# Optimization experiments

Measured on AMD Instinct MI355X. Metric: run time of the kernel, lower is better.

Reference implementation:

```python
import jax, jax.numpy as jnp
import numpy as np

B, T, D, H = 1024, 256, 8, 128


def setup_inputs() -> dict:
    key = jax.random.key(0)
    ks = jax.random.split(key, 8)
    def lin(k, fan_in, fan_out):
        # torch nn.Linear default init: U(-1/sqrt(fan_in), 1/sqrt(fan_in))
        bound = 1.0 / np.sqrt(fan_in)
        return jax.random.uniform(k, (fan_in, fan_out), jnp.float32, -bound, bound)
    return {
        "x": jax.random.normal(ks[0], (B, T, D), jnp.float32),
        "W_in": lin(ks[1], D, H), "b_in": jnp.zeros((H,), jnp.float32),
        "W0": lin(ks[2], H + 1, H), "b0": jnp.zeros((H,), jnp.float32),
        "W1": lin(ks[3], H, H), "b1": jnp.zeros((H,), jnp.float32),
        "W2": lin(ks[4], H, H * D), "b2": jnp.zeros((H * D,), jnp.float32),
    }


def _vector_field(t, z, W0, b0, W1, b1, W2, b2, hidden, inp):
    # inhomogeneous: append scalar time channel -> [B, H+1]
    h = jnp.concatenate([z, jnp.full((z.shape[0], 1), t, z.dtype)], axis=-1)
    h = jax.nn.relu(h @ W0 + b0)
    h = jax.nn.relu(h @ W1 + b1)          # num_layer = 1 extra hidden layer
    return jnp.tanh(h @ W2 + b2).reshape(-1, hidden, inp)  # [B, H, D]


def reference(x, W_in, b_in, W0, b0, W1, b1, W2, b2):
    b, t_len, d = x.shape
    hidden = W_in.shape[1]
    z0 = x[:, 0, :] @ W_in + b_in                     # init_states = input_layer(x[:,0])
    t_grid = jnp.linspace(0.0, 1.0, t_len)
    # linear interpolation of x on t_grid => dX/dt * dt over interval k is x[k+1]-x[k]
    dX = jnp.swapaxes(x[:, 1:, :] - x[:, :-1, :], 0, 1)  # [T-1, B, D]

    def step(z, inp):
        t_k, dx = inp
        F = _vector_field(t_k, z, W0, b0, W1, b1, W2, b2, hidden, d)
        z_next = z + jnp.einsum('bhd,bd->bh', F, dx)  # Euler step
        return z_next, z_next

    _, zs = jax.lax.scan(step, z0, (t_grid[:-1], dX))  # zs: [T-1, B, H]
    return jnp.concatenate([z0[:, None, :], jnp.swapaxes(zs, 0, 1)], axis=1)  # [B, T, H]
```

## Files before the change

### kernel.cpp

```cpp
#include <hip/hip_runtime.h>

#define TLEN 256
#define DD 8
#define HH 128
#define BR 16
#define NTHREADS 512

typedef __attribute__((ext_vector_type(8))) _Float16 half8;
typedef __attribute__((ext_vector_type(4))) float f32x4;

#define LOSCALE 65536.0f
#define LOINV   (1.0f/65536.0f)

static __device__ __forceinline__ float tanh_fast(float x){
  float cx = fminf(fmaxf(x, -9.01f), 9.01f);
  float e = __builtin_amdgcn_exp2f(cx * 2.885390081777927f);
  return 1.0f - 2.0f * __builtin_amdgcn_rcpf(e + 1.0f);
}

static __device__ __forceinline__ void split_store(float v, unsigned short* hiA, unsigned short* loA, unsigned byte){
  _Float16 h = (_Float16)v;
  _Float16 l = (_Float16)(v - (float)h);
  *(_Float16*)((char*)hiA + byte) = h;
  *(_Float16*)((char*)loA + byte) = l;
}

__global__ void pack_w2_kernel(const float* __restrict__ W2, half8* __restrict__ ws){
  int gid = blockIdx.x * 256 + threadIdx.x;
  int l = gid & 63;
  int f = gid >> 6;
  int kt = f & 3, ct = (f >> 2) & 7, w = f >> 5;
  int col = w*128 + ct*16 + (l & 15);
  int kb  = kt*32 + (l >> 4)*8;
  half8 vh, vl;
  #pragma unroll
  for (int j = 0; j < 8; j++){
    float v = W2[(kb + j)*1024 + col];
    _Float16 h = (_Float16)v;
    vh[j] = h;
    vl[j] = (_Float16)((v - (float)h) * LOSCALE);
  }
  ws[f*64 + l] = vh;
  ws[(256 + f)*64 + l] = vl;
}

__global__ __launch_bounds__(NTHREADS, 2) void ncde_kernel(
    const float* __restrict__ x, const float* __restrict__ Win, const float* __restrict__ bin,
    const float* __restrict__ W0, const float* __restrict__ b0v, const float* __restrict__ W1,
    const float* __restrict__ b1v, const float* __restrict__ W2, const float* __restrict__ b2v,
    const half8* __restrict__ wsw2, float* __restrict__ out)
{
  __shared__ half8 w0fh[2048], w0fl[2048];
  __shared__ half8 w1fh[2048], w1fl[2048];
  __shared__ unsigned short zhh[2048], zhl[2048];
  __shared__ unsigned short h1h[2048], h1l[2048];
  __shared__ unsigned short h2h[2048], h2l[2048];
  __shared__ f32x4 b2lds4[256];

  const int t    = threadIdx.x;
  const int lane = t & 63;
  const int w    = t >> 6;
  const int lg   = lane >> 4;
  const int ln   = lane & 15;
  const int b0blk = blockIdx.x * BR;
  const int dbase = (lg & 1) * 4;

  for (int s = t; s < 4096; s += NTHREADS){
    int which = s >> 11;
    int s2 = s & 2047;
    int la = s2 & 63;
    int nt = (s2 >> 6) & 7;
    int kt = s2 >> 9;
    const float* Wsrc = which ? W1 : W0;
    int kb  = kt*32 + (la >> 4)*8;
    int col = nt*16 + (la & 15);
    half8 vh, vl;
    #pragma unroll
    for (int j = 0; j < 8; j++){
      float v = Wsrc[(kb + j)*HH + col];
      _Float16 h = (_Float16)v;
      vh[j] = h;
      vl[j] = (_Float16)((v - (float)h) * LOSCALE);
    }
    if (which){ w1fh[s2] = vh; w1fl[s2] = vl; } else { w0fh[s2] = vh; w0fl[s2] = vl; }
  }
  for (int s = t; s < 1024; s += NTHREADS) ((float*)b2lds4)[s] = b2v[s];

  half8 w2f[8][4];
  #pragma unroll
  for (int ct = 0; ct < 8; ct++)
    #pragma unroll
    for (int kt = 0; kt < 4; kt++)
      w2f[ct][kt] = wsw2[((w*8 + ct)*4 + kt)*64 + lane];
  const half8* wsL = wsw2 + 256*64;

  const float b0r = b0v[w*16 + ln];
  const float w0L = W0[128*HH + w*16 + ln];
  const float b1r = b1v[w*16 + ln];

  f32x4 xprev = *(const f32x4*)(x + (size_t)(b0blk + ln)*(TLEN*DD) + dbase);

  for (int o = t; o < BR*HH; o += NTHREADS){
    int br = o >> 7, h = o & 127;
    float acc = bin[h];
    const float* xb = x + (size_t)(b0blk + br)*(TLEN*DD);
    #pragma unroll
    for (int d = 0; d < DD; d++) acc += xb[d] * Win[d*HH + h];
    unsigned byte = (unsigned)br*256u + (((unsigned)h*2u) ^ (((unsigned)(br & 7)) << 4));
    split_store(acc, zhh, zhl, byte);
  }
  __syncthreads();

  float zreg[8];
  #pragma unroll
  for (int ct = 0; ct < 8; ct++){
    int h = w*16 + ct*2 + (lg >> 1);
    unsigned byte = (unsigned)ln*256u + (((unsigned)h*2u) ^ (((unsigned)(ln & 7)) << 4));
    zreg[ct] = (float)*(_Float16*)((char*)zhh + byte) + (float)*(_Float16*)((char*)zhl + byte);
  }

  float* outp[4];
  #pragma unroll
  for (int i = 0; i < 4; i++){
    int o = t + i*NTHREADS;
    int br = o >> 7, h = o & 127;
    outp[i] = out + (size_t)(b0blk + br)*(TLEN*HH) + h;
    unsigned byte = (unsigned)br*256u + (((unsigned)h*2u) ^ (((unsigned)(br & 7)) << 4));
    *outp[i] = (float)*(_Float16*)((char*)zhh + byte) + (float)*(_Float16*)((char*)zhl + byte);
    outp[i] += HH;
  }

  const float inv = 1.0f / 255.0f;

  for (int k = 0; k < TLEN - 1; k++){
    float tk = (float)k * inv;

    f32x4 xn = *(const f32x4*)(x + (size_t)(b0blk + ln)*(TLEN*DD) + (size_t)(k + 1)*DD + dbase);

    f32x4 acch = {0.f,0.f,0.f,0.f}, accl = {0.f,0.f,0.f,0.f}, acc2 = {0.f,0.f,0.f,0.f};
    #pragma unroll
    for (int kt = 0; kt < 4; kt++){
      unsigned byte = (unsigned)ln*256u + ((((unsigned)(kt*4 + lg))*16u) ^ (((unsigned)(ln & 7)) << 4));
      half8 ahi = *(const half8*)((const char*)zhh + byte);
      half8 alo = *(const half8*)((const char*)zhl + byte);
      half8 bh = w0fh[(kt*8 + w)*64 + lane];
      half8 bl = w0fl[(kt*8 + w)*64 + lane];
      acch = __builtin_amdgcn_mfma_f32_16x16x32_f16(ahi, bh, acch, 0, 0, 0);
      accl = __builtin_amdgcn_mfma_f32_16x16x32_f16(alo, bh, accl, 0, 0, 0);
      acc2 = __builtin_amdgcn_mfma_f32_16x16x32_f16(ahi, bl, acc2, 0, 0, 0);
    }
    {
      float c0 = b0r + tk * w0L;
      #pragma unroll
      for (int r = 0; r < 4; r++){
        float v = fmaxf(acch[r] + accl[r] + acc2[r]*LOINV + c0, 0.0f);
        int row = lg*4 + r;
        unsigned byte = (unsigned)row*256u + ((((unsigned)(w*16 + ln))*2u) ^ (((unsigned)(row & 7)) << 4));
        split_store(v, h1h, h1l, byte);
      }
    }
    __syncthreads();

    acch = (f32x4){0.f,0.f,0.f,0.f}; accl = (f32x4){0.f,0.f,0.f,0.f}; acc2 = (f32x4){0.f,0.f,0.f,0.f};
    #pragma unroll
    for (int kt = 0; kt < 4; kt++){
      unsigned byte = (unsigned)ln*256u + ((((unsigned)(kt*4 + lg))*16u) ^ (((unsigned)(ln & 7)) << 4));
      half8 ahi = *(const half8*)((const char*)h1h + byte);
      half8 alo = *(const half8*)((const char*)h1l + byte);
      half8 bh = w1fh[(kt*8 + w)*64 + lane];
      half8 bl = w1fl[(kt*8 + w)*64 + lane];
      acch = __builtin_amdgcn_mfma_f32_16x16x32_f16(ahi, bh, acch, 0, 0, 0);
      accl = __builtin_amdgcn_mfma_f32_16x16x32_f16(alo, bh, accl, 0, 0, 0);
      acc2 = __builtin_amdgcn_mfma_f32_16x16x32_f16(ahi, bl, acc2, 0, 0, 0);
    }
    #pragma unroll
    for (int r = 0; r < 4; r++){
      float v = fmaxf(acch[r] + accl[r] + acc2[r]*LOINV + b1r, 0.0f);
      int row = lg*4 + r;
      unsigned byte = (unsigned)row*256u + ((((unsigned)(w*16 + ln))*2u) ^ (((unsigned)(row & 7)) << 4));
      split_store(v, h2h, h2l, byte);
    }
    half8 wl[4];
    #pragma unroll
    for (int kt = 0; kt < 4; kt++) wl[kt] = wsL[((w*8 + 0)*4 + kt)*64 + lane];
    __syncthreads();

    half8 ahh[4], ahl[4];
    #pragma unroll
    for (int kt = 0; kt < 4; kt++){
      unsigned byte = (unsigned)ln*256u + ((((unsigned)(kt*4 + lg))*16u) ^ (((unsigned)(ln & 7)) << 4));
      ahh[kt] = *(const half8*)((const char*)h2h + byte);
      ahl[kt] = *(const half8*)((const char*)h2l + byte);
    }
    f32x4 dxr = xn - xprev;
    xprev = xn;

    #pragma unroll
    for (int ct = 0; ct < 8; ct++){
      f32x4 b2q = b2lds4[w*32 + ct*4 + lg];
      f32x4 a3h = {0.f,0.f,0.f,0.f}, a3l = {0.f,0.f,0.f,0.f}, a3c = {0.f,0.f,0.f,0.f};
      #pragma unroll
      for (int kt = 0; kt < 4; kt++)
        a3h = __builtin_amdgcn_mfma_f32_16x16x32_f16(w2f[ct][kt], ahh[kt], a3h, 0, 0, 0);
      #pragma unroll
      for (int kt = 0; kt < 4; kt++)
        a3l = __builtin_amdgcn_mfma_f32_16x16x32_f16(w2f[ct][kt], ahl[kt], a3l, 0, 0, 0);
      #pragma unroll
      for (int kt = 0; kt < 4; kt++)
        a3c = __builtin_amdgcn_mfma_f32_16x16x32_f16(wl[kt], ahh[kt], a3c, 0, 0, 0);
      if (ct < 7){
        #pragma unroll
        for (int kt = 0; kt < 4; kt++) wl[kt] = wsL[((w*8 + ct + 1)*4 + kt)*64 + lane];
      }
      float s = 0.0f;
      #pragma unroll
      for (int r = 0; r < 4; r++){
        float val = tanh_fast(a3h[r] + a3l[r] + a3c[r]*LOINV + b2q[r]);
        s += val * dxr[r];
      }
      s += __shfl_xor(s, 16, 64);
      zreg[ct] += s;
    }

    if ((lg & 1) == 0){
      #pragma unroll
      for (int ct = 0; ct < 8; ct++){
        int h = w*16 + ct*2 + (lg >> 1);
        unsigned byte = (unsigned)ln*256u + (((unsigned)h*2u) ^ (((unsigned)(ln & 7)) << 4));
        split_store(zreg[ct], zhh, zhl, byte);
      }
    }
    __syncthreads();

    #pragma unroll
    for (int i = 0; i < 4; i++){
      int o = t + i*NTHREADS;
      int br = o >> 7, h = o & 127;
      unsigned byte = (unsigned)br*256u + (((unsigned)h*2u) ^ (((unsigned)(br & 7)) << 4));
      *outp[i] = (float)*(_Float16*)((char*)zhh + byte) + (float)*(_Float16*)((char*)zhl + byte);
      outp[i] += HH;
    }
  }
}

extern "C" void kernel_launch(void* const* d_in, const int* in_sizes, int n_in,
                              void* d_out, int out_size, void* d_ws, size_t ws_size,
                              hipStream_t stream) {
  const float* x   = (const float*)d_in[0];
  const float* Win = (const float*)d_in[1];
  const float* bin = (const float*)d_in[2];
  const float* W0  = (const float*)d_in[3];
  const float* b0  = (const float*)d_in[4];
  const float* W1  = (const float*)d_in[5];
  const float* b1  = (const float*)d_in[6];
  const float* W2  = (const float*)d_in[7];
  const float* b2  = (const float*)d_in[8];
  float* out = (float*)d_out;
  half8* wsw2 = (half8*)d_ws;

  pack_w2_kernel<<<dim3(64), dim3(256), 0, stream>>>(W2, wsw2);
  ncde_kernel<<<dim3(1024 / BR), dim3(NTHREADS), 0, stream>>>(
      x, Win, bin, W0, b0, W1, b1, W2, b2, wsw2, out);
}
```

Baseline: 2.250 ms.

## Process two 16-row batch tiles per block with register-resident W0/W1

Each block now handles 32 batch rows as two interleaved 16-row tiles, so the grid shrinks to 32 blocks. The two tiles give independent MFMA chains that can fill pipeline latency in the sequential time loop. W0/W1 hi/lo fragments and b2 are kept in registers instead of LDS, all activations share one swizzled LDS buffer, and the W2 low-part prefetch is double-buffered. In exchange each block does twice the work per step on half as many CUs, and register pressure rises sharply, which risks spills or lower occupancy.

```diff
diff --git a/kernel.cpp b/kernel.cpp
--- a/kernel.cpp
+++ b/kernel.cpp
@@ -3,7 +3,6 @@
 #define TLEN 256
 #define DD 8
 #define HH 128
-#define BR 16
 #define NTHREADS 512
 
 typedef __attribute__((ext_vector_type(8))) _Float16 half8;
@@ -11,18 +10,12 @@
 
 #define LOSCALE 65536.0f
 #define LOINV   (1.0f/65536.0f)
+#define TSTRIDE 24576
 
 static __device__ __forceinline__ float tanh_fast(float x){
   float cx = fminf(fmaxf(x, -9.01f), 9.01f);
   float e = __builtin_amdgcn_exp2f(cx * 2.885390081777927f);
   return 1.0f - 2.0f * __builtin_amdgcn_rcpf(e + 1.0f);
-}
-
-static __device__ __forceinline__ void split_store(float v, unsigned short* hiA, unsigned short* loA, unsigned byte){
-  _Float16 h = (_Float16)v;
-  _Float16 l = (_Float16)(v - (float)h);
-  *(_Float16*)((char*)hiA + byte) = h;
-  *(_Float16*)((char*)loA + byte) = l;
 }
 
 __global__ void pack_w2_kernel(const float* __restrict__ W2, half8* __restrict__ ws){
@@ -50,41 +43,30 @@
     const float* __restrict__ b1v, const float* __restrict__ W2, const float* __restrict__ b2v,
     const half8* __restrict__ wsw2, float* __restrict__ out)
 {
-  __shared__ half8 w0fh[2048], w0fl[2048];
-  __shared__ half8 w1fh[2048], w1fl[2048];
-  __shared__ unsigned short zhh[2048], zhl[2048];
-  __shared__ unsigned short h1h[2048], h1l[2048];
-  __shared__ unsigned short h2h[2048], h2l[2048];
-  __shared__ f32x4 b2lds4[256];
+  __shared__ unsigned short act[2*6*2048];
 
   const int t    = threadIdx.x;
   const int lane = t & 63;
   const int w    = t >> 6;
   const int lg   = lane >> 4;
   const int ln   = lane & 15;
-  const int b0blk = blockIdx.x * BR;
+  const int b0blk = blockIdx.x * 32;
   const int dbase = (lg & 1) * 4;
 
-  for (int s = t; s < 4096; s += NTHREADS){
-    int which = s >> 11;
-    int s2 = s & 2047;
-    int la = s2 & 63;
-    int nt = (s2 >> 6) & 7;
-    int kt = s2 >> 9;
-    const float* Wsrc = which ? W1 : W0;
-    int kb  = kt*32 + (la >> 4)*8;
-    int col = nt*16 + (la & 15);
-    half8 vh, vl;
+  half8 w0h[4], w0l[4], w1h[4], w1l[4];
+  #pragma unroll
+  for (int kt = 0; kt < 4; kt++){
+    half8 vh, vl, uh, ul;
     #pragma unroll
     for (int j = 0; j < 8; j++){
-      float v = Wsrc[(kb + j)*HH + col];
-      _Float16 h = (_Float16)v;
-      vh[j] = h;
-      vl[j] = (_Float16)((v - (float)h) * LOSCALE);
-    }
-    if (which){ w1fh[s2] = vh; w1fl[s2] = vl; } else { w0fh[s2] = vh; w0fl[s2] = vl; }
-  }
-  for (int s = t; s < 1024; s += NTHREADS) ((float*)b2lds4)[s] = b2v[s];
+      int krow = kt*32 + (lane >> 4)*8 + j;
+      float v0 = W0[krow*HH + w*16 + ln];
+      _Float16 h0 = (_Float16)v0; vh[j] = h0; vl[j] = (_Float16)((v0 - (float)h0)*LOSCALE);
+      float v1 = W1[krow*HH + w*16 + ln];
+      _Float16 h1 = (_Float16)v1; uh[j] = h1; ul[j] = (_Float16)((v1 - (float)h1)*LOSCALE);
+    }
+    w0h[kt] = vh; w0l[kt] = vl; w1h[kt] = uh; w1l[kt] = ul;
+  }
 
   half8 w2f[8][4];
   #pragma unroll
@@ -97,148 +79,202 @@
   const float b0r = b0v[w*16 + ln];
   const float w0L = W0[128*HH + w*16 + ln];
   const float b1r = b1v[w*16 + ln];
-
-  f32x4 xprev = *(const f32x4*)(x + (size_t)(b0blk + ln)*(TLEN*DD) + dbase);
-
-  for (int o = t; o < BR*HH; o += NTHREADS){
-    int br = o >> 7, h = o & 127;
-    float acc = bin[h];
-    const float* xb = x + (size_t)(b0blk + br)*(TLEN*DD);
-    #pragma unroll
-    for (int d = 0; d < DD; d++) acc += xb[d] * Win[d*HH + h];
-    unsigned byte = (unsigned)br*256u + (((unsigned)h*2u) ^ (((unsigned)(br & 7)) << 4));
-    split_store(acc, zhh, zhl, byte);
-  }
-  __syncthreads();
-
-  float zreg[8];
+  f32x4 b2r4[8];
+  #pragma unroll
+  for (int ct = 0; ct < 8; ct++)
+    b2r4[ct] = *(const f32x4*)(b2v + w*128 + ct*16 + lg*4);
+
+  unsigned ard[4];
+  #pragma unroll
+  for (int kt = 0; kt < 4; kt++)
+    ard[kt] = (unsigned)ln*256u + (((unsigned)(kt*64 + lg*16)) ^ (((unsigned)(ln & 7)) << 4));
+  unsigned sst[4];
+  #pragma unroll
+  for (int r = 0; r < 4; r++){
+    int row = lg*4 + r;
+    sst[r] = (unsigned)row*256u + ((((unsigned)(w*16 + ln))*2u) ^ (((unsigned)(row & 7)) << 4));
+  }
+  unsigned zst[8];
   #pragma unroll
   for (int ct = 0; ct < 8; ct++){
     int h = w*16 + ct*2 + (lg >> 1);
-    unsigned byte = (unsigned)ln*256u + (((unsigned)h*2u) ^ (((unsigned)(ln & 7)) << 4));
-    zreg[ct] = (float)*(_Float16*)((char*)zhh + byte) + (float)*(_Float16*)((char*)zhl + byte);
-  }
-
-  float* outp[4];
-  #pragma unroll
-  for (int i = 0; i < 4; i++){
+    zst[ct] = (unsigned)ln*256u + (((unsigned)h*2u) ^ (((unsigned)(ln & 7)) << 4));
+  }
+  unsigned ovr[8]; unsigned orow[8];
+  #pragma unroll
+  for (int i = 0; i < 8; i++){
     int o = t + i*NTHREADS;
-    int br = o >> 7, h = o & 127;
-    outp[i] = out + (size_t)(b0blk + br)*(TLEN*HH) + h;
-    unsigned byte = (unsigned)br*256u + (((unsigned)h*2u) ^ (((unsigned)(br & 7)) << 4));
-    *outp[i] = (float)*(_Float16*)((char*)zhh + byte) + (float)*(_Float16*)((char*)zhl + byte);
-    outp[i] += HH;
-  }
+    int br = o >> 7, h = o & 127, brt = br & 15;
+    ovr[i]  = (unsigned)(br >> 4)*TSTRIDE + (unsigned)brt*256u +
+              (((unsigned)h*2u) ^ (((unsigned)(brt & 7)) << 4));
+    orow[i] = (unsigned)(b0blk + br)*(TLEN*HH) + (unsigned)h;
+  }
+
+  const float* xb0 = x + (size_t)(b0blk + ln)*(TLEN*DD) + dbase;
+  const float* xb1 = x + (size_t)(b0blk + 16 + ln)*(TLEN*DD) + dbase;
+  f32x4 xprev0 = *(const f32x4*)xb0;
+  f32x4 xprev1 = *(const f32x4*)xb1;
+
+  for (int o = t; o < 4096; o += NTHREADS){
+    int br = o >> 7, h = o & 127, brt = br & 15;
+    float acc = bin[h];
+    const float* xr = x + (size_t)(b0blk + br)*(TLEN*DD);
+    #pragma unroll
+    for (int d = 0; d < DD; d++) acc += xr[d] * Win[d*HH + h];
+    unsigned byte = (unsigned)(br >> 4)*TSTRIDE + (unsigned)brt*256u +
+                    (((unsigned)h*2u) ^ (((unsigned)(brt & 7)) << 4));
+    _Float16 hv = (_Float16)acc;
+    *(_Float16*)((char*)act + byte)        = hv;
+    *(_Float16*)((char*)act + byte + 4096) = (_Float16)(acc - (float)hv);
+  }
+  __syncthreads();
+
+  float zreg[2][8];
+  #pragma unroll
+  for (int g = 0; g < 2; g++)
+    #pragma unroll
+    for (int ct = 0; ct < 8; ct++){
+      unsigned byte = zst[ct] + g*TSTRIDE;
+      zreg[g][ct] = (float)*(_Float16*)((char*)act + byte)
+                  + (float)*(_Float16*)((char*)act + byte + 4096);
+    }
+
+  #pragma unroll
+  for (int i = 0; i < 8; i++)
+    out[orow[i]] = (float)*(_Float16*)((char*)act + ovr[i])
+                 + (float)*(_Float16*)((char*)act + ovr[i] + 4096);
 
   const float inv = 1.0f / 255.0f;
 
   for (int k = 0; k < TLEN - 1; k++){
     float tk = (float)k * inv;
 
-    f32x4 xn = *(const f32x4*)(x + (size_t)(b0blk + ln)*(TLEN*DD) + (size_t)(k + 1)*DD + dbase);
-
-    f32x4 acch = {0.f,0.f,0.f,0.f}, accl = {0.f,0.f,0.f,0.f}, acc2 = {0.f,0.f,0.f,0.f};
-    #pragma unroll
-    for (int kt = 0; kt < 4; kt++){
-      unsigned byte = (unsigned)ln*256u + ((((unsigned)(kt*4 + lg))*16u) ^ (((unsigned)(ln & 7)) << 4));
-      half8 ahi = *(const half8*)((const char*)zhh + byte);
-      half8 alo = *(const half8*)((const char*)zhl + byte);
-      half8 bh = w0fh[(kt*8 + w)*64 + lane];
-      half8 bl = w0fl[(kt*8 + w)*64 + lane];
-      acch = __builtin_amdgcn_mfma_f32_16x16x32_f16(ahi, bh, acch, 0, 0, 0);
-      accl = __builtin_amdgcn_mfma_f32_16x16x32_f16(alo, bh, accl, 0, 0, 0);
-      acc2 = __builtin_amdgcn_mfma_f32_16x16x32_f16(ahi, bl, acc2, 0, 0, 0);
-    }
+    f32x4 xn0 = *(const f32x4*)(xb0 + (size_t)(k + 1)*DD);
+    f32x4 xn1 = *(const f32x4*)(xb1 + (size_t)(k + 1)*DD);
+
     {
+      f32x4 ah0={0,0,0,0}, al0={0,0,0,0}, ac0={0,0,0,0};
+      f32x4 ah1={0,0,0,0}, al1={0,0,0,0}, ac1={0,0,0,0};
+      #pragma unroll
+      for (int kt = 0; kt < 4; kt++){
+        half8 zh0 = *(const half8*)((const char*)act + ard[kt]);
+        half8 zl0 = *(const half8*)((const char*)act + ard[kt] + 4096);
+        half8 zh1 = *(const half8*)((const char*)act + ard[kt] + TSTRIDE);
+        half8 zl1 = *(const half8*)((const char*)act + ard[kt] + TSTRIDE + 4096);
+        ah0 = __builtin_amdgcn_mfma_f32_16x16x32_f16(zh0, w0h[kt], ah0, 0, 0, 0);
+        ah1 = __builtin_amdgcn_mfma_f32_16x16x32_f16(zh1, w0h[kt], ah1, 0, 0, 0);
+        al0 = __builtin_amdgcn_mfma_f32_16x16x32_f16(zl0, w0h[kt], al0, 0, 0, 0);
+        al1 = __builtin_amdgcn_mfma_f32_16x16x32_f16(zl1, w0h[kt], al1, 0, 0, 0);
+        ac0 = __builtin_amdgcn_mfma_f32_16x16x32_f16(zh0, w0l[kt], ac0, 0, 0, 0);
+        ac1 = __builtin_amdgcn_mfma_f32_16x16x32_f16(zh1, w0l[kt], ac1, 0, 0, 0);
+      }
       float c0 = b0r + tk * w0L;
       #pragma unroll
       for (int r = 0; r < 4; r++){
-        float v = fmaxf(acch[r] + accl[r] + acc2[r]*LOINV + c0, 0.0f);
-        int row = lg*4 + r;
-        unsigned byte = (unsigned)row*256u + ((((unsigned)(w*16 + ln))*2u) ^ (((unsigned)(row & 7)) << 4));
-        split_store(v, h1h, h1l, byte);
+        float v0 = fmaxf(ah0[r] + al0[r] + ac0[r]*LOINV + c0, 0.0f);
+        float v1 = fmaxf(ah1[r] + al1[r] + ac1[r]*LOINV + c0, 0.0f);
+        _Float16 h0 = (_Float16)v0, h1 = (_Float16)v1;
+        *(_Float16*)((char*)act + sst[r] + 2*4096)            = h0;
+        *(_Float16*)((char*)act + sst[r] + 3*4096)            = (_Float16)(v0 - (float)h0);
+        *(_Float16*)((char*)act + sst[r] + TSTRIDE + 2*4096)  = h1;
+        *(_Float16*)((char*)act + sst[r] + TSTRIDE + 3*4096)  = (_Float16)(v1 - (float)h1);
       }
     }
     __syncthreads();
 
-    acch = (f32x4){0.f,0.f,0.f,0.f}; accl = (f32x4){0.f,0.f,0.f,0.f}; acc2 = (f32x4){0.f,0.f,0.f,0.f};
-    #pragma unroll
-    for (int kt = 0; kt < 4; kt++){
-      unsigned byte = (unsigned)ln*256u + ((((unsigned)(kt*4 + lg))*16u) ^ (((unsigned)(ln & 7)) << 4));
-      half8 ahi = *(const half8*)((const char*)h1h + byte);
-      half8 alo = *(const half8*)((const char*)h1l + byte);
-      half8 bh = w1fh[(kt*8 + w)*64 + lane];
-      half8 bl = w1fl[(kt*8 + w)*64 + lane];
-      acch = __builtin_amdgcn_mfma_f32_16x16x32_f16(ahi, bh, acch, 0, 0, 0);
-      accl = __builtin_amdgcn_mfma_f32_16x16x32_f16(alo, bh, accl, 0, 0, 0);
-      acc2 = __builtin_amdgcn_mfma_f32_16x16x32_f16(ahi, bl, acc2, 0, 0, 0);
-    }
-    #pragma unroll
-    for (int r = 0; r < 4; r++){
-      float v = fmaxf(acch[r] + accl[r] + acc2[r]*LOINV + b1r, 0.0f);
-      int row = lg*4 + r;
-      unsigned byte = (unsigned)row*256u + ((((unsigned)(w*16 + ln))*2u) ^ (((unsigned)(row & 7)) << 4));
-      split_store(v, h2h, h2l, byte);
-    }
-    half8 wl[4];
-    #pragma unroll
-    for (int kt = 0; kt < 4; kt++) wl[kt] = wsL[((w*8 + 0)*4 + kt)*64 + lane];
+    {
+      f32x4 ah0={0,0,0,0}, al0={0,0,0,0}, ac0={0,0,0,0};
+      f32x4 ah1={0,0,0,0}, al1={0,0,0,0}, ac1={0,0,0,0};
+      #pragma unroll
+      for (int kt = 0; kt < 4; kt++){
+        half8 zh0 = *(const half8*)((const char*)act + ard[kt] + 2*4096);
+        half8 zl0 = *(const half8*)((const char*)act + ard[kt] + 3*4096);
+        half8 zh1 = *(const half8*)((const char*)act + ard[kt] + TSTRIDE + 2*4096);
+        half8 zl1 = *(const half8*)((const char*)act + ard[kt] + TSTRIDE + 3*4096);
+        ah0 = __builtin_amdgcn_mfma_f32_16x16x32_f16(zh0, w1h[kt], ah0, 0, 0, 0);
+        ah1 = __builtin_amdgcn_mfma_f32_16x16x32_f16(zh1, w1h[kt], ah1, 0, 0, 0);
+        al0 = __builtin_amdgcn_mfma_f32_16x16x32_f16(zl0, w1h[kt], al0, 0, 0, 0);
+        al1 = __builtin_amdgcn_mfma_f32_16x16x32_f16(zl1, w1h[kt], al1, 0, 0, 0);
+        ac0 = __builtin_amdgcn_mfma_f32_16x16x32_f16(zh0, w1l[kt], ac0, 0, 0, 0);
+        ac1 = __builtin_amdgcn_mfma_f32_16x16x32_f16(zh1, w1l[kt], ac1, 0, 0, 0);
+      }
+      #pragma unroll
+      for (int r = 0; r < 4; r++){
+        float v0 = fmaxf(ah0[r] + al0[r] + ac0[r]*LOINV + b1r, 0.0f);
+        float v1 = fmaxf(ah1[r] + al1[r] + ac1[r]*LOINV + b1r, 0.0f);
+        _Float16 h0 = (_Float16)v0, h1 = (_Float16)v1;
+        *(_Float16*)((char*)act + sst[r] + 4*4096)            = h0;
+        *(_Float16*)((char*)act + sst[r] + 5*4096)            = (_Float16)(v0 - (float)h0);
+        *(_Float16*)((char*)act + sst[r] + TSTRIDE + 4*4096)  = h1;
+        *(_Float16*)((char*)act + sst[r] + TSTRIDE + 5*4096)  = (_Float16)(v1 - (float)h1);
+      }
+    }
+    half8 wl[2][4];
+    #pragma unroll
+    for (int kt = 0; kt < 4; kt++) wl[0][kt] = wsL[((w*8 + 0)*4 + kt)*64 + lane];
     __syncthreads();
 
-    half8 ahh[4], ahl[4];
-    #pragma unroll
-    for (int kt = 0; kt < 4; kt++){
-      unsigned byte = (unsigned)ln*256u + ((((unsigned)(kt*4 + lg))*16u) ^ (((unsigned)(ln & 7)) << 4));
-      ahh[kt] = *(const half8*)((const char*)h2h + byte);
-      ahl[kt] = *(const half8*)((const char*)h2l + byte);
-    }
-    f32x4 dxr = xn - xprev;
-    xprev = xn;
+    half8 ahh[2][4], ahl[2][4];
+    #pragma unroll
+    for (int g = 0; g < 2; g++)
+      #pragma unroll
+      for (int kt = 0; kt < 4; kt++){
+        ahh[g][kt] = *(const half8*)((const char*)act + ard[kt] + g*TSTRIDE + 4*4096);
+        ahl[g][kt] = *(const half8*)((const char*)act + ard[kt] + g*TSTRIDE + 5*4096);
+      }
+    f32x4 dxr0 = xn0 - xprev0; xprev0 = xn0;
+    f32x4 dxr1 = xn1 - xprev1; xprev1 = xn1;
 
     #pragma unroll
     for (int ct = 0; ct < 8; ct++){
-      f32x4 b2q = b2lds4[w*32 + ct*4 + lg];
-      f32x4 a3h = {0.f,0.f,0.f,0.f}, a3l = {0.f,0.f,0.f,0.f}, a3c = {0.f,0.f,0.f,0.f};
-      #pragma unroll
-      for (int kt = 0; kt < 4; kt++)
-        a3h = __builtin_amdgcn_mfma_f32_16x16x32_f16(w2f[ct][kt], ahh[kt], a3h, 0, 0, 0);
-      #pragma unroll
-      for (int kt = 0; kt < 4; kt++)
-        a3l = __builtin_amdgcn_mfma_f32_16x16x32_f16(w2f[ct][kt], ahl[kt], a3l, 0, 0, 0);
-      #pragma unroll
-      for (int kt = 0; kt < 4; kt++)
-        a3c = __builtin_amdgcn_mfma_f32_16x16x32_f16(wl[kt], ahh[kt], a3c, 0, 0, 0);
       if (ct < 7){
         #pragma unroll
-        for (int kt = 0; kt < 4; kt++) wl[kt] = wsL[((w*8 + ct + 1)*4 + kt)*64 + lane];
-      }
-      float s = 0.0f;
+        for (int kt = 0; kt < 4; kt++)
+          wl[(ct + 1) & 1][kt] = wsL[((w*8 + ct + 1)*4 + kt)*64 + lane];
+      }
+      f32x4 h30={0,0,0,0}, l30={0,0,0,0}, c30={0,0,0,0};
+      f32x4 h31={0,0,0,0}, l31={0,0,0,0}, c31={0,0,0,0};
+      #pragma unroll
+      for (int kt = 0; kt < 4; kt++){
+        h30 = __builtin_amdgcn_mfma_f32_16x16x32_f16(w2f[ct][kt], ahh[0][kt], h30, 0, 0, 0);
+        h31 = __builtin_amdgcn_mfma_f32_16x16x32_f16(w2f[ct][kt], ahh[1][kt], h31, 0, 0, 0);
+        l30 = __builtin_amdgcn_mfma_f32_16x16x32_f16(w2f[ct][kt], ahl[0][kt], l30, 0, 0, 0);
+        l31 = __builtin_amdgcn_mfma_f32_16x16x32_f16(w2f[ct][kt], ahl[1][kt], l31, 0, 0, 0);
+        c30 = __builtin_amdgcn_mfma_f32_16x16x32_f16(wl[ct & 1][kt], ahh[0][kt], c30, 0, 0, 0);
+        c31 = __builtin_amdgcn_mfma_f32_16x16x32_f16(wl[ct & 1][kt], ahh[1][kt], c31, 0, 0, 0);
+      }
+      float s0 = 0.0f, s1 = 0.0f;
       #pragma unroll
       for (int r = 0; r < 4; r++){
-        float val = tanh_fast(a3h[r] + a3l[r] + a3c[r]*LOINV + b2q[r]);
-        s += val * dxr[r];
-      }
-      s += __shfl_xor(s, 16, 64);
-      zreg[ct] += s;
+        s0 += tanh_fast(h30[r] + l30[r] + c30[r]*LOINV + b2r4[ct][r]) * dxr0[r];
+        s1 += tanh_fast(h31[r] + l31[r] + c31[r]*LOINV + b2r4[ct][r]) * dxr1[r];
+      }
+      s0 += __shfl_xor(s0, 16, 64);
+      s1 += __shfl_xor(s1, 16, 64);
+      zreg[0][ct] += s0;
+      zreg[1][ct] += s1;
     }
 
     if ((lg & 1) == 0){
       #pragma unroll
-      for (int ct = 0; ct < 8; ct++){
-        int h = w*16 + ct*2 + (lg >> 1);
-        unsigned byte = (unsigned)ln*256u + (((unsigned)h*2u) ^ (((unsigned)(ln & 7)) << 4));
-        split_store(zreg[ct], zhh, zhl, byte);
-      }
+      for (int g = 0; g < 2; g++)
+        #pragma unroll
+        for (int ct = 0; ct < 8; ct++){
+          float v = zreg[g][ct];
+          _Float16 hv = (_Float16)v;
+          unsigned byte = zst[ct] + g*TSTRIDE;
+          *(_Float16*)((char*)act + byte)        = hv;
+          *(_Float16*)((char*)act + byte + 4096) = (_Float16)(v - (float)hv);
+        }
     }
     __syncthreads();
 
-    #pragma unroll
-    for (int i = 0; i < 4; i++){
-      int o = t + i*NTHREADS;
-      int br = o >> 7, h = o & 127;
-      unsigned byte = (unsigned)br*256u + (((unsigned)h*2u) ^ (((unsigned)(br & 7)) << 4));
-      *outp[i] = (float)*(_Float16*)((char*)zhh + byte) + (float)*(_Float16*)((char*)zhl + byte);
-      outp[i] += HH;
+    {
+      float* outk = out + (size_t)(k + 1)*HH;
+      #pragma unroll
+      for (int i = 0; i < 8; i++)
+        outk[orow[i]] = (float)*(_Float16*)((char*)act + ovr[i])
+                      + (float)*(_Float16*)((char*)act + ovr[i] + 4096);
     }
   }
 }
@@ -259,6 +295,6 @@
   half8* wsw2 = (half8*)d_ws;
 
   pack_w2_kernel<<<dim3(64), dim3(256), 0, stream>>>(W2, wsw2);
-  ncde_kernel<<<dim3(1024 / BR), dim3(NTHREADS), 0, stream>>>(
+  ncde_kernel<<<dim3(32), dim3(NTHREADS), 0, stream>>>(
       x, Win, bin, W0, b0, W1, b1, W2, b2, wsw2, out);
 }
```

Measured after the change: 4.588 ms. 2.04x slower.

## Double block to 16 waves, split W2 layer across all waves, specialize output writers

Applied to the files above, without the earlier changes.

The block grows from 8 to 16 wavefronts for the same 16 batch rows. The 1024-column W2 GEMM is now split across all 16 waves (4 column tiles each instead of 8). The idle upper 8 waves write the previous step's z to global memory while the lower 8 compute the first hidden layer. W2 fragments are streamed from global/L2 each step instead of being held in registers, which frees VGPRs but adds per-step memory traffic; the W2 section also gets a raised s_setprio.

```diff
diff --git a/kernel.cpp b/kernel.cpp
--- a/kernel.cpp
+++ b/kernel.cpp
@@ -3,8 +3,7 @@
 #define TLEN 256
 #define DD 8
 #define HH 128
-#define BR 16
-#define NTHREADS 512
+#define NT 1024
 
 typedef __attribute__((ext_vector_type(8))) _Float16 half8;
 typedef __attribute__((ext_vector_type(4))) float f32x4;
@@ -18,19 +17,12 @@
   return 1.0f - 2.0f * __builtin_amdgcn_rcpf(e + 1.0f);
 }
 
-static __device__ __forceinline__ void split_store(float v, unsigned short* hiA, unsigned short* loA, unsigned byte){
-  _Float16 h = (_Float16)v;
-  _Float16 l = (_Float16)(v - (float)h);
-  *(_Float16*)((char*)hiA + byte) = h;
-  *(_Float16*)((char*)loA + byte) = l;
-}
-
 __global__ void pack_w2_kernel(const float* __restrict__ W2, half8* __restrict__ ws){
   int gid = blockIdx.x * 256 + threadIdx.x;
   int l = gid & 63;
   int f = gid >> 6;
-  int kt = f & 3, ct = (f >> 2) & 7, w = f >> 5;
-  int col = w*128 + ct*16 + (l & 15);
+  int kt = f & 3, c16 = f >> 2;
+  int col = c16*16 + (l & 15);
   int kb  = kt*32 + (l >> 4)*8;
   half8 vh, vl;
   #pragma unroll
@@ -44,7 +36,7 @@
   ws[(256 + f)*64 + l] = vl;
 }
 
-__global__ __launch_bounds__(NTHREADS, 2) void ncde_kernel(
+__global__ __launch_bounds__(NT, 4) void ncde_kernel(
     const float* __restrict__ x, const float* __restrict__ Win, const float* __restrict__ bin,
     const float* __restrict__ W0, const float* __restrict__ b0v, const float* __restrict__ W1,
     const float* __restrict__ b1v, const float* __restrict__ W2, const float* __restrict__ b2v,
@@ -52,20 +44,19 @@
 {
   __shared__ half8 w0fh[2048], w0fl[2048];
   __shared__ half8 w1fh[2048], w1fl[2048];
-  __shared__ unsigned short zhh[2048], zhl[2048];
-  __shared__ unsigned short h1h[2048], h1l[2048];
-  __shared__ unsigned short h2h[2048], h2l[2048];
-  __shared__ f32x4 b2lds4[256];
+  __shared__ unsigned short act[6*2048];
+  __shared__ float b2lds[1024];
 
   const int t    = threadIdx.x;
   const int lane = t & 63;
-  const int w    = t >> 6;
+  const int q    = t >> 6;
   const int lg   = lane >> 4;
   const int ln   = lane & 15;
-  const int b0blk = blockIdx.x * BR;
+  const int b0blk = blockIdx.x * 16;
   const int dbase = (lg & 1) * 4;
-
-  for (int s = t; s < 4096; s += NTHREADS){
+  char* const actc = (char*)act;
+
+  for (int s = t; s < 4096; s += NT){
     int which = s >> 11;
     int s2 = s & 2047;
     int la = s2 & 63;
@@ -80,166 +71,174 @@
       float v = Wsrc[(kb + j)*HH + col];
       _Float16 h = (_Float16)v;
       vh[j] = h;
-      vl[j] = (_Float16)((v - (float)h) * LOSCALE);
+      vl[j] = (_Float16)((v - (float)h)*LOSCALE);
     }
     if (which){ w1fh[s2] = vh; w1fl[s2] = vl; } else { w0fh[s2] = vh; w0fl[s2] = vl; }
   }
-  for (int s = t; s < 1024; s += NTHREADS) ((float*)b2lds4)[s] = b2v[s];
-
-  half8 w2f[8][4];
-  #pragma unroll
-  for (int ct = 0; ct < 8; ct++)
-    #pragma unroll
-    for (int kt = 0; kt < 4; kt++)
-      w2f[ct][kt] = wsw2[((w*8 + ct)*4 + kt)*64 + lane];
+  for (int s = t; s < 1024; s += NT) b2lds[s] = b2v[s];
+
   const half8* wsL = wsw2 + 256*64;
 
-  const float b0r = b0v[w*16 + ln];
-  const float w0L = W0[128*HH + w*16 + ln];
-  const float b1r = b1v[w*16 + ln];
-
-  f32x4 xprev = *(const f32x4*)(x + (size_t)(b0blk + ln)*(TLEN*DD) + dbase);
-
-  for (int o = t; o < BR*HH; o += NTHREADS){
+  const float b0r = b0v[(q & 7)*16 + ln];
+  const float w0L = W0[128*HH + (q & 7)*16 + ln];
+  const float b1r = b1v[(q & 7)*16 + ln];
+
+  unsigned ard[4];
+  #pragma unroll
+  for (int kt = 0; kt < 4; kt++)
+    ard[kt] = (unsigned)ln*256u + (((unsigned)(kt*64 + lg*16)) ^ (((unsigned)(ln & 7)) << 4));
+  unsigned sst[4];
+  #pragma unroll
+  for (int r = 0; r < 4; r++){
+    int row = lg*4 + r;
+    sst[r] = (unsigned)row*256u + ((((unsigned)((q & 7)*16 + ln))*2u) ^ (((unsigned)(row & 7)) << 4));
+  }
+  unsigned zst[4];
+  #pragma unroll
+  for (int j = 0; j < 4; j++){
+    int h = q*8 + j*2 + (lg >> 1);
+    zst[j] = (unsigned)ln*256u + (((unsigned)h*2u) ^ (((unsigned)(ln & 7)) << 4));
+  }
+
+  const float* xb = x + (size_t)(b0blk + ln)*(TLEN*DD) + dbase;
+  f32x4 xprev = *(const f32x4*)xb;
+
+  for (int o = t; o < 2048; o += NT){
     int br = o >> 7, h = o & 127;
     float acc = bin[h];
-    const float* xb = x + (size_t)(b0blk + br)*(TLEN*DD);
-    #pragma unroll
-    for (int d = 0; d < DD; d++) acc += xb[d] * Win[d*HH + h];
+    const float* xr = x + (size_t)(b0blk + br)*(TLEN*DD);
+    #pragma unroll
+    for (int d = 0; d < DD; d++) acc += xr[d] * Win[d*HH + h];
     unsigned byte = (unsigned)br*256u + (((unsigned)h*2u) ^ (((unsigned)(br & 7)) << 4));
-    split_store(acc, zhh, zhl, byte);
+    _Float16 hv = (_Float16)acc;
+    *(_Float16*)(actc + byte)        = hv;
+    *(_Float16*)(actc + byte + 4096) = (_Float16)(acc - (float)hv);
   }
   __syncthreads();
 
-  float zreg[8];
-  #pragma unroll
-  for (int ct = 0; ct < 8; ct++){
-    int h = w*16 + ct*2 + (lg >> 1);
-    unsigned byte = (unsigned)ln*256u + (((unsigned)h*2u) ^ (((unsigned)(ln & 7)) << 4));
-    zreg[ct] = (float)*(_Float16*)((char*)zhh + byte) + (float)*(_Float16*)((char*)zhl + byte);
-  }
-
-  float* outp[4];
-  #pragma unroll
-  for (int i = 0; i < 4; i++){
-    int o = t + i*NTHREADS;
+  float zreg[4];
+  #pragma unroll
+  for (int j = 0; j < 4; j++)
+    zreg[j] = (float)*(_Float16*)(actc + zst[j])
+            + (float)*(_Float16*)(actc + zst[j] + 4096);
+
+  for (int k = 0; k < TLEN - 1; k++){
+    float tk = (float)k * (1.0f/255.0f);
+    f32x4 xn = *(const f32x4*)(xb + (size_t)(k + 1)*DD);
+
+    if (q < 8){
+      f32x4 ah = {0,0,0,0}, al = {0,0,0,0}, ac = {0,0,0,0};
+      #pragma unroll
+      for (int kt = 0; kt < 4; kt++){
+        half8 zh_ = *(const half8*)(actc + ard[kt]);
+        half8 zl_ = *(const half8*)(actc + ard[kt] + 4096);
+        half8 bh = w0fh[(kt*8 + q)*64 + lane];
+        half8 bl = w0fl[(kt*8 + q)*64 + lane];
+        ah = __builtin_amdgcn_mfma_f32_16x16x32_f16(zh_, bh, ah, 0, 0, 0);
+        al = __builtin_amdgcn_mfma_f32_16x16x32_f16(zl_, bh, al, 0, 0, 0);
+        ac = __builtin_amdgcn_mfma_f32_16x16x32_f16(zh_, bl, ac, 0, 0, 0);
+      }
+      float c0 = b0r + tk * w0L;
+      #pragma unroll
+      for (int r = 0; r < 4; r++){
+        float v = fmaxf(ah[r] + al[r] + ac[r]*LOINV + c0, 0.0f);
+        _Float16 hv = (_Float16)v;
+        *(_Float16*)(actc + sst[r] + 2*4096) = hv;
+        *(_Float16*)(actc + sst[r] + 3*4096) = (_Float16)(v - (float)hv);
+      }
+    } else {
+      #pragma unroll
+      for (int i = 0; i < 4; i++){
+        int o = (t - 512) + i*512;
+        int br = o >> 7, h = o & 127;
+        unsigned byte = (unsigned)br*256u + (((unsigned)h*2u) ^ (((unsigned)(br & 7)) << 4));
+        float val = (float)*(_Float16*)(actc + byte)
+                  + (float)*(_Float16*)(actc + byte + 4096);
+        out[(size_t)(b0blk + br)*(TLEN*HH) + (size_t)k*HH + h] = val;
+      }
+    }
+    __syncthreads();
+
+    if (q < 8){
+      f32x4 ah = {0,0,0,0}, al = {0,0,0,0}, ac = {0,0,0,0};
+      #pragma unroll
+      for (int kt = 0; kt < 4; kt++){
+        half8 zh_ = *(const half8*)(actc + ard[kt] + 2*4096);
+        half8 zl_ = *(const half8*)(actc + ard[kt] + 3*4096);
+        half8 bh = w1fh[(kt*8 + q)*64 + lane];
+        half8 bl = w1fl[(kt*8 + q)*64 + lane];
+        ah = __builtin_amdgcn_mfma_f32_16x16x32_f16(zh_, bh, ah, 0, 0, 0);
+        al = __builtin_amdgcn_mfma_f32_16x16x32_f16(zl_, bh, al, 0, 0, 0);
+        ac = __builtin_amdgcn_mfma_f32_16x16x32_f16(zh_, bl, ac, 0, 0, 0);
+      }
+      #pragma unroll
+      for (int r = 0; r < 4; r++){
+        float v = fmaxf(ah[r] + al[r] + ac[r]*LOINV + b1r, 0.0f);
+        _Float16 hv = (_Float16)v;
+        *(_Float16*)(actc + sst[r] + 4*4096) = hv;
+        *(_Float16*)(actc + sst[r] + 5*4096) = (_Float16)(v - (float)hv);
+      }
+    }
+    half8 wh[4], wlo[4];
+    #pragma unroll
+    for (int kt = 0; kt < 4; kt++){
+      wh[kt]  = wsw2[(q*16 + kt)*64 + lane];
+      wlo[kt] = wsL [(q*16 + kt)*64 + lane];
+    }
+    __syncthreads();
+
+    f32x4 dxr = xn - xprev; xprev = xn;
+    float sacc[4];
+    __builtin_amdgcn_s_setprio(1);
+    #pragma unroll
+    for (int j = 0; j < 4; j++){
+      f32x4 hh = {0,0,0,0}, hl = {0,0,0,0}, hc = {0,0,0,0};
+      #pragma unroll
+      for (int kt = 0; kt < 4; kt++){
+        half8 ah_ = *(const half8*)(actc + ard[kt] + 4*4096);
+        half8 al_ = *(const half8*)(actc + ard[kt] + 5*4096);
+        hh = __builtin_amdgcn_mfma_f32_16x16x32_f16(wh[kt],  ah_, hh, 0, 0, 0);
+        hl = __builtin_amdgcn_mfma_f32_16x16x32_f16(wh[kt],  al_, hl, 0, 0, 0);
+        hc = __builtin_amdgcn_mfma_f32_16x16x32_f16(wlo[kt], ah_, hc, 0, 0, 0);
+      }
+      if (j < 3){
+        #pragma unroll
+        for (int kt = 0; kt < 4; kt++){
+          wh[kt]  = wsw2[(q*16 + (j + 1)*4 + kt)*64 + lane];
+          wlo[kt] = wsL [(q*16 + (j + 1)*4 + kt)*64 + lane];
+        }
+      }
+      f32x4 b2q = *(const f32x4*)&b2lds[q*64 + j*16 + lg*4];
+      float s = 0.0f;
+      #pragma unroll
+      for (int r = 0; r < 4; r++)
+        s += tanh_fast(hh[r] + hl[r] + hc[r]*LOINV + b2q[r]) * dxr[r];
+      sacc[j] = s;
+    }
+    __builtin_amdgcn_s_setprio(0);
+
+    #pragma unroll
+    for (int j = 0; j < 4; j++){
+      sacc[j] += __shfl_xor(sacc[j], 16, 64);
+      zreg[j] += sacc[j];
+    }
+    if ((lg & 1) == 0){
+      #pragma unroll
+      for (int j = 0; j < 4; j++){
+        float v = zreg[j];
+        _Float16 hv = (_Float16)v;
+        *(_Float16*)(actc + zst[j])        = hv;
+        *(_Float16*)(actc + zst[j] + 4096) = (_Float16)(v - (float)hv);
+      }
+    }
+    __syncthreads();
+  }
+
+  for (int o = t; o < 2048; o += NT){
     int br = o >> 7, h = o & 127;
-    outp[i] = out + (size_t)(b0blk + br)*(TLEN*HH) + h;
     unsigned byte = (unsigned)br*256u + (((unsigned)h*2u) ^ (((unsigned)(br & 7)) << 4));
-    *outp[i] = (float)*(_Float16*)((char*)zhh + byte) + (float)*(_Float16*)((char*)zhl + byte);
-    outp[i] += HH;
-  }
-
-  const float inv = 1.0f / 255.0f;
-
-  for (int k = 0; k < TLEN - 1; k++){
-    float tk = (float)k * inv;
-
-    f32x4 xn = *(const f32x4*)(x + (size_t)(b0blk + ln)*(TLEN*DD) + (size_t)(k + 1)*DD + dbase);
-
-    f32x4 acch = {0.f,0.f,0.f,0.f}, accl = {0.f,0.f,0.f,0.f}, acc2 = {0.f,0.f,0.f,0.f};
-    #pragma unroll
-    for (int kt = 0; kt < 4; kt++){
-      unsigned byte = (unsigned)ln*256u + ((((unsigned)(kt*4 + lg))*16u) ^ (((unsigned)(ln & 7)) << 4));
-      half8 ahi = *(const half8*)((const char*)zhh + byte);
-      half8 alo = *(const half8*)((const char*)zhl + byte);
-      half8 bh = w0fh[(kt*8 + w)*64 + lane];
-      half8 bl = w0fl[(kt*8 + w)*64 + lane];
-      acch = __builtin_amdgcn_mfma_f32_16x16x32_f16(ahi, bh, acch, 0, 0, 0);
-      accl = __builtin_amdgcn_mfma_f32_16x16x32_f16(alo, bh, accl, 0, 0, 0);
-      acc2 = __builtin_amdgcn_mfma_f32_16x16x32_f16(ahi, bl, acc2, 0, 0, 0);
-    }
-    {
-      float c0 = b0r + tk * w0L;
-      #pragma unroll
-      for (int r = 0; r < 4; r++){
-        float v = fmaxf(acch[r] + accl[r] + acc2[r]*LOINV + c0, 0.0f);
-        int row = lg*4 + r;
-        unsigned byte = (unsigned)row*256u + ((((unsigned)(w*16 + ln))*2u) ^ (((unsigned)(row & 7)) << 4));
-        split_store(v, h1h, h1l, byte);
-      }
-    }
-    __syncthreads();
-
-    acch = (f32x4){0.f,0.f,0.f,0.f}; accl = (f32x4){0.f,0.f,0.f,0.f}; acc2 = (f32x4){0.f,0.f,0.f,0.f};
-    #pragma unroll
-    for (int kt = 0; kt < 4; kt++){
-      unsigned byte = (unsigned)ln*256u + ((((unsigned)(kt*4 + lg))*16u) ^ (((unsigned)(ln & 7)) << 4));
-      half8 ahi = *(const half8*)((const char*)h1h + byte);
-      half8 alo = *(const half8*)((const char*)h1l + byte);
-      half8 bh = w1fh[(kt*8 + w)*64 + lane];
-      half8 bl = w1fl[(kt*8 + w)*64 + lane];
-      acch = __builtin_amdgcn_mfma_f32_16x16x32_f16(ahi, bh, acch, 0, 0, 0);
-      accl = __builtin_amdgcn_mfma_f32_16x16x32_f16(alo, bh, accl, 0, 0, 0);
-      acc2 = __builtin_amdgcn_mfma_f32_16x16x32_f16(ahi, bl, acc2, 0, 0, 0);
-    }
-    #pragma unroll
-    for (int r = 0; r < 4; r++){
-      float v = fmaxf(acch[r] + accl[r] + acc2[r]*LOINV + b1r, 0.0f);
-      int row = lg*4 + r;
-      unsigned byte = (unsigned)row*256u + ((((unsigned)(w*16 + ln))*2u) ^ (((unsigned)(row & 7)) << 4));
-      split_store(v, h2h, h2l, byte);
-    }
-    half8 wl[4];
-    #pragma unroll
-    for (int kt = 0; kt < 4; kt++) wl[kt] = wsL[((w*8 + 0)*4 + kt)*64 + lane];
-    __syncthreads();
-
-    half8 ahh[4], ahl[4];
-    #pragma unroll
-    for (int kt = 0; kt < 4; kt++){
-      unsigned byte = (unsigned)ln*256u + ((((unsigned)(kt*4 + lg))*16u) ^ (((unsigned)(ln & 7)) << 4));
-      ahh[kt] = *(const half8*)((const char*)h2h + byte);
-      ahl[kt] = *(const half8*)((const char*)h2l + byte);
-    }
-    f32x4 dxr = xn - xprev;
-    xprev = xn;
-
-    #pragma unroll
-    for (int ct = 0; ct < 8; ct++){
-      f32x4 b2q = b2lds4[w*32 + ct*4 + lg];
-      f32x4 a3h = {0.f,0.f,0.f,0.f}, a3l = {0.f,0.f,0.f,0.f}, a3c = {0.f,0.f,0.f,0.f};
-      #pragma unroll
-      for (int kt = 0; kt < 4; kt++)
-        a3h = __builtin_amdgcn_mfma_f32_16x16x32_f16(w2f[ct][kt], ahh[kt], a3h, 0, 0, 0);
-      #pragma unroll
-      for (int kt = 0; kt < 4; kt++)
-        a3l = __builtin_amdgcn_mfma_f32_16x16x32_f16(w2f[ct][kt], ahl[kt], a3l, 0, 0, 0);
-      #pragma unroll
-      for (int kt = 0; kt < 4; kt++)
-        a3c = __builtin_amdgcn_mfma_f32_16x16x32_f16(wl[kt], ahh[kt], a3c, 0, 0, 0);
-      if (ct < 7){
-        #pragma unroll
-        for (int kt = 0; kt < 4; kt++) wl[kt] = wsL[((w*8 + ct + 1)*4 + kt)*64 + lane];
-      }
-      float s = 0.0f;
-      #pragma unroll
-      for (int r = 0; r < 4; r++){
-        float val = tanh_fast(a3h[r] + a3l[r] + a3c[r]*LOINV + b2q[r]);
-        s += val * dxr[r];
-      }
-      s += __shfl_xor(s, 16, 64);
-      zreg[ct] += s;
-    }
-
-    if ((lg & 1) == 0){
-      #pragma unroll
-      for (int ct = 0; ct < 8; ct++){
-        int h = w*16 + ct*2 + (lg >> 1);
-        unsigned byte = (unsigned)ln*256u + (((unsigned)h*2u) ^ (((unsigned)(ln & 7)) << 4));
-        split_store(zreg[ct], zhh, zhl, byte);
-      }
-    }
-    __syncthreads();
-
-    #pragma unroll
-    for (int i = 0; i < 4; i++){
-      int o = t + i*NTHREADS;
-      int br = o >> 7, h = o & 127;
-      unsigned byte = (unsigned)br*256u + (((unsigned)h*2u) ^ (((unsigned)(br & 7)) << 4));
-      *outp[i] = (float)*(_Float16*)((char*)zhh + byte) + (float)*(_Float16*)((char*)zhl + byte);
-      outp[i] += HH;
-    }
+    out[(size_t)(b0blk + br)*(TLEN*HH) + (size_t)(TLEN - 1)*HH + h] =
+        (float)*(_Float16*)(actc + byte) + (float)*(_Float16*)(actc + byte + 4096);
   }
 }
 
@@ -259,6 +258,6 @@
   half8* wsw2 = (half8*)d_ws;
 
   pack_w2_kernel<<<dim3(64), dim3(256), 0, stream>>>(W2, wsw2);
-  ncde_kernel<<<dim3(1024 / BR), dim3(NTHREADS), 0, stream>>>(
+  ncde_kernel<<<dim3(64), dim3(NT), 0, stream>>>(
       x, Win, bin, W0, b0, W1, b1, W2, b2, wsw2, out);
 }
```

New measurement: 5.250 ms. 133% more time.
